# Performance work log

Hardware: AMD Instinct MI355X
Metric: run time of the kernel (lower is better)

The kernel has to match this reference:

```python
import jax, jax.numpy as jnp
import numpy as np

N_PARTICLES = 10_000_000
GRID_N = 256  # per-axis grid size
GRID_EDGE = 10.0  # grid spans [-10, 10] in each axis


def setup_inputs() -> dict:
    key = jax.random.key(0)
    k1, k2 = jax.random.split(key)
    # uniform in [-11, 11]: some particles fall outside the grid -> exercises bounds mask
    positions = jax.random.uniform(k1, (N_PARTICLES, 3), dtype=jnp.float32,
                                   minval=-11.0, maxval=11.0)
    weights = jax.random.uniform(k2, (N_PARTICLES,), dtype=jnp.float32)
    return {"positions": positions, "weights": weights}


def reference(positions, weights):
    # Grid buffers (from Grid.__init__ with grid_edges=(10,10,10), n=(256,256,256))
    n = GRID_N
    grid_min = jnp.full((3,), -GRID_EDGE, dtype=positions.dtype)
    grid_max = jnp.full((3,), GRID_EDGE, dtype=positions.dtype)
    dx = (grid_max - grid_min) / (n - 1)  # [3]

    # float index: fi = (pos - min)/dx  -> nearest grid point via trunc(fi + 0.5)
    fi = (positions - grid_min[None, :]) / dx[None, :]          # [N,3]
    i = (fi + 0.5).astype(jnp.int32)  # C-style trunc-toward-zero, matches torch .type(int64)

    gd = jnp.all((i >= 0) & (i < n), axis=1)                    # [N] in-grid mask

    # flatten 3D index; out-of-grid particles routed to index 0 with zero weight
    flat = (i[:, 0] * n + i[:, 1]) * n + i[:, 2]                # [N]
    flat = jnp.where(gd, flat, 0)
    w = jnp.where(gd, weights, jnp.zeros_like(weights))

    grid = jnp.zeros((n * n * n,), dtype=positions.dtype).at[flat].add(w)
    return grid.reshape(n, n, n)
```

## Files before the change

kernel.cpp:

```cpp
#include <hip/hip_runtime.h>
#include <stdint.h>


constexpr int GRID_N = 256;
constexpr int SB     = 1024;
constexpr int CELLS  = 16384;
constexpr int NB     = 256;
constexpr int BT     = 1024;
constexpr int RING   = 16;
constexpr int RSTR   = 17;
constexpr uint32_t SIDE_CAP = 65536;

typedef unsigned int u32x4 __attribute__((ext_vector_type(4)));
typedef float        f32x4 __attribute__((ext_vector_type(4)));

#define BAR_LGKM() do { \
    asm volatile("s_waitcnt lgkmcnt(0)" ::: "memory"); \
    __builtin_amdgcn_s_barrier(); \
} while (0)

__device__ __forceinline__ int particle_flat(float px, float py, float pz) {
#pragma clang fp contract(off)
    float fix = (px + 10.0f) * 12.75f;
    float fiy = (py + 10.0f) * 12.75f;
    float fiz = (pz + 10.0f) * 12.75f;
    int ix = (int)(fix + 0.5f);
    int iy = (int)(fiy + 0.5f);
    int iz = (int)(fiz + 0.5f);
    bool in = (ix >= 0) & (ix < GRID_N) &
              (iy >= 0) & (iy < GRID_N) &
              (iz >= 0) & (iz < GRID_N);
    return in ? ((ix << 16) | (iy << 8) | iz) : -1;
}

__global__ __launch_bounds__(1024) void k0_init(uint32_t* __restrict__ gcur,
                                                uint32_t* __restrict__ side_n,
                                                uint32_t C)
{
    int t = blockIdx.x * blockDim.x + threadIdx.x;
    if (t < SB) gcur[t] = (uint32_t)t * C;
    if (t == 0) *side_n = 0;
}

__global__ __launch_bounds__(BT, 1) void k3_direct(
    const float* __restrict__ pos, const float* __restrict__ wgt,
    uint32_t* __restrict__ gcur, uint2* __restrict__ pairs,
    uint2* __restrict__ side, uint32_t* __restrict__ side_n,
    uint32_t C, int n)
{
    __shared__ uint2    stg[SB][RSTR];
    __shared__ uint32_t s_total[SB];
    __shared__ uint32_t s_flushed[SB];
    __shared__ uint32_t s_wl[SB];
    __shared__ uint32_t s_wldst[SB];
    __shared__ uint32_t s_wln;

    const int tid = threadIdx.x;
    const int blk = blockIdx.x;

    s_total[tid]   = 0;
    s_flushed[tid] = 0;
    if (tid == 0) s_wln = 0;
    __syncthreads();

    const float4* p4 = (const float4*)pos;
    const float4* w4 = (const float4*)wgt;
    int ngroups = n >> 2;
    int G = NB * BT;
    int iters = (ngroups + G - 1) / G;

    int g = blk * BT + tid;
    bool valid = g < ngroups;
    float4 a = {}, b = {}, c = {}, w = {};
    if (valid) {
        a = p4[(size_t)g * 3 + 0];
        b = p4[(size_t)g * 3 + 1];
        c = p4[(size_t)g * 3 + 2];
        w = w4[g];
    }

    for (int it = 0; it < iters; ++it) {
        if (tid == 0) s_wln = 0;

        int gn = g + G;
        bool v2 = (it + 1 < iters) && (gn < ngroups);
        float4 a2 = {}, b2 = {}, c2 = {}, w2 = {};
        if (v2) {
            a2 = p4[(size_t)gn * 3 + 0];
            b2 = p4[(size_t)gn * 3 + 1];
            c2 = p4[(size_t)gn * 3 + 2];
            w2 = w4[gn];
        }

        if (valid) {
            int   f[4]  = { particle_flat(a.x, a.y, a.z), particle_flat(a.w, b.x, b.y),
                            particle_flat(b.z, b.w, c.x), particle_flat(c.y, c.z, c.w) };
            float ww[4] = { w.x, w.y, w.z, w.w };
#pragma unroll
            for (int k = 0; k < 4; ++k) {
                int fk = f[k];
                if (fk >= 0) {
                    uint32_t bin  = (uint32_t)fk >> 14;
                    uint32_t slot = atomicAdd(&s_total[bin], 1u);
                    if (slot - s_flushed[bin] < (uint32_t)RING) {
                        stg[bin][slot & (RING - 1)] =
                            make_uint2((uint32_t)fk & (CELLS - 1), __float_as_uint(ww[k]));
                    } else {
                        atomicSub(&s_total[bin], 1u);
                        uint32_t si = atomicAdd(side_n, 1u);
                        if (si < SIDE_CAP)
                            side[si] = make_uint2((uint32_t)fk, __float_as_uint(ww[k]));
                    }
                }
            }
        }
        BAR_LGKM();
        {
            uint32_t p = s_total[tid] - s_flushed[tid];
            if (p >= 8u) {
                uint32_t o   = s_flushed[tid];
                uint32_t dst = atomicAdd(&gcur[tid], 8u);
                if (dst + 8u <= (uint32_t)(tid + 1) * C) {
                    uint32_t wi = atomicAdd(&s_wln, 1u);
                    s_wl[wi]    = ((uint32_t)tid << 4) | (o & (RING - 1));
                    s_wldst[wi] = dst;
                } else {
                    atomicSub(&gcur[tid], 8u);
                    for (int j = 0; j < 8; ++j) {
                        uint2 v = stg[tid][(o + j) & (RING - 1)];
                        uint32_t si = atomicAdd(side_n, 1u);
                        if (si < SIDE_CAP)
                            side[si] = make_uint2(((uint32_t)tid << 14) | v.x, v.y);
                    }
                }
                s_flushed[tid] = o + 8u;
            }
        }
        BAR_LGKM();
        {
            uint32_t m = s_wln;
            for (uint32_t j = tid; j < m * 8u; j += BT) {
                uint32_t e = s_wl[j >> 3];
                uint2 v = stg[e >> 4][((e & (RING - 1)) + (j & 7u)) & (RING - 1)];
                uint64_t v64 = (uint64_t)v.x | ((uint64_t)v.y << 32);
                __builtin_nontemporal_store(v64,
                    (uint64_t*)&pairs[(size_t)s_wldst[j >> 3] + (j & 7u)]);
            }
        }
        BAR_LGKM();

        a = a2; b = b2; c = c2; w = w2; valid = v2; g = gn;
    }

    if (blk == 0 && tid == 0) {
        for (int p = n & ~3; p < n; ++p) {
            int f = particle_flat(pos[3 * p], pos[3 * p + 1], pos[3 * p + 2]);
            if (f >= 0) {
                uint32_t si = atomicAdd(side_n, 1u);
                if (si < SIDE_CAP)
                    side[si] = make_uint2((uint32_t)f, __float_as_uint(wgt[p]));
            }
        }
    }

    {
        uint32_t t = s_total[tid];
        uint32_t p = t - s_flushed[tid];
        uint32_t pad = ((p + 7u) & ~7u) - p;
        for (uint32_t j = 0; j < pad; ++j)
            stg[tid][(t + j) & (RING - 1)] = make_uint2(0u, 0u);
        s_total[tid] = t + pad;
    }
    __syncthreads();

    for (int r = 0; r < 2; ++r) {
        if (tid == 0) s_wln = 0;
        __syncthreads();
        {
            uint32_t p = s_total[tid] - s_flushed[tid];
            if (p >= 8u) {
                uint32_t o   = s_flushed[tid];
                uint32_t dst = atomicAdd(&gcur[tid], 8u);
                if (dst + 8u <= (uint32_t)(tid + 1) * C) {
                    uint32_t wi = atomicAdd(&s_wln, 1u);
                    s_wl[wi]    = ((uint32_t)tid << 4) | (o & (RING - 1));
                    s_wldst[wi] = dst;
                } else {
                    atomicSub(&gcur[tid], 8u);
                    for (int j = 0; j < 8; ++j) {
                        uint2 v = stg[tid][(o + j) & (RING - 1)];
                        uint32_t si = atomicAdd(side_n, 1u);
                        if (si < SIDE_CAP)
                            side[si] = make_uint2(((uint32_t)tid << 14) | v.x, v.y);
                    }
                }
                s_flushed[tid] = o + 8u;
            }
        }
        __syncthreads();
        {
            uint32_t m = s_wln;
            for (uint32_t j = tid; j < m * 8u; j += BT) {
                uint32_t e = s_wl[j >> 3];
                uint2 v = stg[e >> 4][((e & (RING - 1)) + (j & 7u)) & (RING - 1)];
                uint64_t v64 = (uint64_t)v.x | ((uint64_t)v.y << 32);
                __builtin_nontemporal_store(v64,
                    (uint64_t*)&pairs[(size_t)s_wldst[j >> 3] + (j & 7u)]);
            }
        }
        __syncthreads();
    }
}

__global__ __launch_bounds__(BT) void k4_direct(const uint2* __restrict__ pairs,
                                                const uint32_t* __restrict__ gcur,
                                                const uint2* __restrict__ side,
                                                const uint32_t* __restrict__ side_n,
                                                uint32_t C,
                                                float* __restrict__ grid)
{
    __shared__ float acc[CELLS];
    for (int i = threadIdx.x; i < CELLS; i += BT) acc[i] = 0.0f;
    __syncthreads();

    int b = blockIdx.x;
    uint32_t s = (uint32_t)b * C, e = gcur[b];
    const u32x4* pp = (const u32x4*)(pairs + s);
    uint32_t m = (e - s) >> 1;
    for (uint32_t i = threadIdx.x; i < m; i += BT) {
        u32x4 v = __builtin_nontemporal_load(&pp[i]);
        atomicAdd(&acc[v.x], __uint_as_float(v.y));
        atomicAdd(&acc[v.z], __uint_as_float(v.w));
    }
    uint32_t ns = *side_n;
    if (ns > SIDE_CAP) ns = SIDE_CAP;
    for (uint32_t i = threadIdx.x; i < ns; i += BT) {
        uint2 sv = side[i];
        if ((int)(sv.x >> 14) == b)
            atomicAdd(&acc[sv.x & (CELLS - 1)], __uint_as_float(sv.y));
    }
    __syncthreads();

    f32x4* out4 = (f32x4*)(grid + (size_t)b * CELLS);
    const f32x4* a4 = (const f32x4*)acc;
    for (int i = threadIdx.x; i < CELLS / 4; i += BT)
        __builtin_nontemporal_store(a4[i], &out4[i]);
}

__global__ __launch_bounds__(BT) void k1_hist(const float* __restrict__ pos,
                                              uint32_t* __restrict__ hist,
                                              int n)
{
    __shared__ uint32_t h[SB];
    for (int i = threadIdx.x; i < SB; i += BT) h[i] = 0;
    __syncthreads();

    const float4* p4 = (const float4*)pos;
    int ngroups = n >> 2;
    int G = gridDim.x * BT;
    for (int g = blockIdx.x * BT + threadIdx.x; g < ngroups; g += G) {
        float4 a = p4[(size_t)g * 3 + 0];
        float4 b = p4[(size_t)g * 3 + 1];
        float4 c = p4[(size_t)g * 3 + 2];
        int f0 = particle_flat(a.x, a.y, a.z);
        int f1 = particle_flat(a.w, b.x, b.y);
        int f2 = particle_flat(b.z, b.w, c.x);
        int f3 = particle_flat(c.y, c.z, c.w);
        if (f0 >= 0) atomicAdd(&h[f0 >> 14], 1u);
        if (f1 >= 0) atomicAdd(&h[f1 >> 14], 1u);
        if (f2 >= 0) atomicAdd(&h[f2 >> 14], 1u);
        if (f3 >= 0) atomicAdd(&h[f3 >> 14], 1u);
    }
    if (blockIdx.x == 0 && threadIdx.x == 0) {
        for (int p = n & ~3; p < n; ++p) {
            int f = particle_flat(pos[3 * p], pos[3 * p + 1], pos[3 * p + 2]);
            if (f >= 0) atomicAdd(&h[f >> 14], 1u);
        }
    }
    __syncthreads();
    uint32_t* out = hist + (size_t)blockIdx.x * SB;
    for (int i = threadIdx.x; i < SB; i += BT) out[i] = h[i];
}

__global__ __launch_bounds__(128) void k2a_colscan(const uint32_t* __restrict__ hist,
                                                   uint32_t* __restrict__ offs,
                                                   uint32_t* __restrict__ totals)
{
    int b = blockIdx.x * 128 + threadIdx.x;
    uint32_t run = 0;
    for (int blk = 0; blk < NB; blk += 8) {
        uint32_t v[8];
#pragma unroll
        for (int j = 0; j < 8; ++j)
            v[j] = hist[(size_t)(blk + j) * SB + b];
#pragma unroll
        for (int j = 0; j < 8; ++j) {
            offs[(size_t)(blk + j) * SB + b] = run;
            run += v[j];
        }
    }
    totals[b] = run;
}

__global__ __launch_bounds__(256) void k2b_scan(const uint32_t* __restrict__ totals,
                                                uint32_t* __restrict__ base)
{
    __shared__ uint32_t part[256];
    int t = threadIdx.x;
    uint32_t local[4];
    uint32_t s = 0;
#pragma unroll
    for (int j = 0; j < 4; ++j) { local[j] = totals[t * 4 + j]; s += local[j]; }
    part[t] = s;
    __syncthreads();
    if (t == 0) {
        uint32_t run = 0;
        for (int i = 0; i < 256; ++i) { uint32_t tmp = part[i]; part[i] = run; run += tmp; }
    }
    __syncthreads();
    uint32_t run = part[t];
#pragma unroll
    for (int j = 0; j < 4; ++j) { base[t * 4 + j] = run; run += local[j]; }
    if (t == 255) base[SB] = run;
}

__global__ __launch_bounds__(BT) void k3_scatter(const float* __restrict__ pos,
                                                 const float* __restrict__ wgt,
                                                 const uint32_t* __restrict__ offs,
                                                 const uint32_t* __restrict__ base,
                                                 uint2* __restrict__ pairs,
                                                 int n)
{
    __shared__ uint32_t cur[SB];
    for (int i = threadIdx.x; i < SB; i += BT)
        cur[i] = base[i] + offs[(size_t)blockIdx.x * SB + i];
    __syncthreads();

    const float4* p4 = (const float4*)pos;
    const float4* w4 = (const float4*)wgt;
    int ngroups = n >> 2;
    int G = gridDim.x * BT;
    for (int g = blockIdx.x * BT + threadIdx.x; g < ngroups; g += G) {
        float4 a = p4[(size_t)g * 3 + 0];
        float4 b = p4[(size_t)g * 3 + 1];
        float4 c = p4[(size_t)g * 3 + 2];
        float4 w = w4[g];
        int   f[4]  = { particle_flat(a.x, a.y, a.z), particle_flat(a.w, b.x, b.y),
                        particle_flat(b.z, b.w, c.x), particle_flat(c.y, c.z, c.w) };
        float ww[4] = { w.x, w.y, w.z, w.w };
#pragma unroll
        for (int k = 0; k < 4; ++k) {
            if (f[k] >= 0) {
                uint32_t slot = atomicAdd(&cur[f[k] >> 14], 1u);
                pairs[slot] = make_uint2((uint32_t)(f[k] & (CELLS - 1)),
                                         __float_as_uint(ww[k]));
            }
        }
    }
    if (blockIdx.x == 0 && threadIdx.x == 0) {
        for (int p = n & ~3; p < n; ++p) {
            int f = particle_flat(pos[3 * p], pos[3 * p + 1], pos[3 * p + 2]);
            if (f >= 0) {
                uint32_t slot = atomicAdd(&cur[f >> 14], 1u);
                pairs[slot] = make_uint2((uint32_t)(f & (CELLS - 1)),
                                         __float_as_uint(wgt[p]));
            }
        }
    }
}

__global__ __launch_bounds__(BT) void k4_seg(const uint2* __restrict__ pairs,
                                             const uint32_t* __restrict__ base,
                                             float* __restrict__ grid)
{
    __shared__ float acc[CELLS];
    for (int i = threadIdx.x; i < CELLS; i += BT) acc[i] = 0.0f;
    __syncthreads();

    int b = blockIdx.x;
    uint32_t s = base[b], e = base[b + 1];
    for (uint32_t i = s + threadIdx.x; i < e; i += BT) {
        uint2 p = pairs[i];
        atomicAdd(&acc[p.x], __uint_as_float(p.y));
    }
    __syncthreads();

    float4* out4 = (float4*)(grid + (size_t)b * CELLS);
    const float4* a4 = (const float4*)acc;
    for (int i = threadIdx.x; i < CELLS / 4; i += BT) out4[i] = a4[i];
}

__global__ __launch_bounds__(256) void forcegrid_scatter_atomic(
    const float* __restrict__ pos, const float* __restrict__ wgt,
    float* __restrict__ grid, int n)
{
    int t = blockIdx.x * blockDim.x + threadIdx.x;
    long long bse = (long long)t * 4;
    if (bse >= n) return;
    const float4* p4 = (const float4*)pos;
    float4 a = p4[(size_t)t * 3 + 0];
    float4 b = p4[(size_t)t * 3 + 1];
    float4 c = p4[(size_t)t * 3 + 2];
    float4 w = ((const float4*)wgt)[t];
    int   f[4]  = { particle_flat(a.x, a.y, a.z), particle_flat(a.w, b.x, b.y),
                    particle_flat(b.z, b.w, c.x), particle_flat(c.y, c.z, c.w) };
    float ww[4] = { w.x, w.y, w.z, w.w };
#pragma unroll
    for (int k = 0; k < 4; ++k) {
        if (bse + k >= n) break;
        if (f[k] >= 0) atomicAdd(&grid[f[k]], ww[k]);
    }
}

extern "C" void kernel_launch(void* const* d_in, const int* in_sizes, int n_in,
                              void* d_out, int out_size, void* d_ws, size_t ws_size,
                              hipStream_t stream)
{
    const float* pos = (const float*)d_in[0];
    const float* wgt = (const float*)d_in[1];
    float* grid = (float*)d_out;
    int n = in_sizes[0] / 3;

    uint32_t C = ((2u * (uint32_t)(n / SB) + 4096u) + 7u) & ~7u;
    if (C < 1024u) C = 1024u;
    size_t o1 = 0;
    uint2*    pairs1 = (uint2*)d_ws;                     o1 += (size_t)SB * C * sizeof(uint2);
    uint2*    side   = (uint2*)((char*)d_ws + o1);       o1 += (size_t)SIDE_CAP * sizeof(uint2);
    uint32_t* gcur   = (uint32_t*)((char*)d_ws + o1);    o1 += (size_t)SB * 4;
    uint32_t* side_n = (uint32_t*)((char*)d_ws + o1);    o1 += 64;

    if (ws_size >= o1) {
        k0_init  <<<1,  1024, 0, stream>>>(gcur, side_n, C);
        k3_direct<<<NB, BT,   0, stream>>>(pos, wgt, gcur, pairs1, side, side_n, C, n);
        k4_direct<<<SB, BT,   0, stream>>>(pairs1, gcur, side, side_n, C, grid);
        return;
    }

    size_t o2 = 0;
    uint2*    pairs2  = (uint2*)d_ws;                    o2 += (size_t)n * sizeof(uint2);
    uint32_t* hist2   = (uint32_t*)((char*)d_ws + o2);   o2 += (size_t)NB * SB * 4;
    uint32_t* offs2   = (uint32_t*)((char*)d_ws + o2);   o2 += (size_t)NB * SB * 4;
    uint32_t* totals2 = (uint32_t*)((char*)d_ws + o2);   o2 += (size_t)SB * 4;
    uint32_t* base2   = (uint32_t*)((char*)d_ws + o2);   o2 += (size_t)(SB + 1) * 4;

    if (ws_size >= o2) {
        k1_hist    <<<NB,       BT,  0, stream>>>(pos, hist2, n);
        k2a_colscan<<<SB / 128, 128, 0, stream>>>(hist2, offs2, totals2);
        k2b_scan   <<<1,        256, 0, stream>>>(totals2, base2);
        k3_scatter <<<NB,       BT,  0, stream>>>(pos, wgt, offs2, base2, pairs2, n);
        k4_seg     <<<SB,       BT,  0, stream>>>(pairs2, base2, grid);
    } else {
        (void)hipMemsetAsync(grid, 0, (size_t)out_size * sizeof(float), stream);
        int groups = (n + 3) / 4;
        forcegrid_scatter_atomic<<<(groups + 255) / 256, 256, 0, stream>>>(pos, wgt, grid, n);
    }
}
```

Measured before the change: 297.7 us.

## Use fixed per-(bin,block) pair segments instead of global atomic cursors

Each binning block now writes its staged pairs for each bin into a private fixed-capacity segment indexed by (bin, block), so no global atomic cursor is needed. Each thread flushes its own bin's ring directly with four 16-byte nontemporal stores, which removes the worklist and one barrier per iteration. Bin counts go to a cnt array that the accumulate kernel reads to walk its 256 segments, four threads per segment. Any overflow past CAP entries goes to the side buffer. This gives up compact contiguous segments, so the accumulate reads become more fragmented, and skewed inputs may spill heavily to the capped side list.

```diff
diff --git a/kernel.cpp b/kernel.cpp
--- a/kernel.cpp
+++ b/kernel.cpp
@@ -9,6 +9,7 @@
 constexpr int BT     = 1024;
 constexpr int RING   = 16;
 constexpr int RSTR   = 17;
+constexpr uint32_t CAP = 72;
 constexpr uint32_t SIDE_CAP = 65536;
 
 typedef unsigned int u32x4 __attribute__((ext_vector_type(4)));
@@ -33,35 +34,28 @@
     return in ? ((ix << 16) | (iy << 8) | iz) : -1;
 }
 
-__global__ __launch_bounds__(1024) void k0_init(uint32_t* __restrict__ gcur,
-                                                uint32_t* __restrict__ side_n,
-                                                uint32_t C)
-{
-    int t = blockIdx.x * blockDim.x + threadIdx.x;
-    if (t < SB) gcur[t] = (uint32_t)t * C;
-    if (t == 0) *side_n = 0;
+__global__ __launch_bounds__(64) void k0_init(uint32_t* __restrict__ side_n)
+{
+    if (threadIdx.x == 0) *side_n = 0;
 }
 
 __global__ __launch_bounds__(BT, 1) void k3_direct(
     const float* __restrict__ pos, const float* __restrict__ wgt,
-    uint32_t* __restrict__ gcur, uint2* __restrict__ pairs,
-    uint2* __restrict__ side, uint32_t* __restrict__ side_n,
-    uint32_t C, int n)
+    uint2* __restrict__ pairs, uint32_t* __restrict__ cnt,
+    uint2* __restrict__ side, uint32_t* __restrict__ side_n, int n)
 {
     __shared__ uint2    stg[SB][RSTR];
     __shared__ uint32_t s_total[SB];
     __shared__ uint32_t s_flushed[SB];
-    __shared__ uint32_t s_wl[SB];
-    __shared__ uint32_t s_wldst[SB];
-    __shared__ uint32_t s_wln;
 
     const int tid = threadIdx.x;
     const int blk = blockIdx.x;
 
     s_total[tid]   = 0;
     s_flushed[tid] = 0;
-    if (tid == 0) s_wln = 0;
-    __syncthreads();
+    __syncthreads();
+
+    const size_t segbase = ((size_t)tid * NB + blk) * CAP;
 
     const float4* p4 = (const float4*)pos;
     const float4* w4 = (const float4*)wgt;
@@ -80,8 +74,6 @@
     }
 
     for (int it = 0; it < iters; ++it) {
-        if (tid == 0) s_wln = 0;
-
         int gn = g + G;
         bool v2 = (it + 1 < iters) && (gn < ngroups);
         float4 a2 = {}, b2 = {}, c2 = {}, w2 = {};
@@ -116,36 +108,35 @@
         }
         BAR_LGKM();
         {
-            uint32_t p = s_total[tid] - s_flushed[tid];
-            if (p >= 8u) {
-                uint32_t o   = s_flushed[tid];
-                uint32_t dst = atomicAdd(&gcur[tid], 8u);
-                if (dst + 8u <= (uint32_t)(tid + 1) * C) {
-                    uint32_t wi = atomicAdd(&s_wln, 1u);
-                    s_wl[wi]    = ((uint32_t)tid << 4) | (o & (RING - 1));
-                    s_wldst[wi] = dst;
+            uint32_t t_ = s_total[tid];
+            uint32_t fl = s_flushed[tid];
+            while (t_ - fl >= 8u) {
+                uint32_t o = fl & (RING - 1);
+                if (fl < CAP) {
+                    uint2 v0 = stg[tid][o + 0], v1 = stg[tid][o + 1];
+                    uint2 v2r = stg[tid][o + 2], v3 = stg[tid][o + 3];
+                    uint2 v4 = stg[tid][o + 4], v5 = stg[tid][o + 5];
+                    uint2 v6 = stg[tid][o + 6], v7 = stg[tid][o + 7];
+                    u32x4 q0 = { v0.x, v0.y, v1.x, v1.y };
+                    u32x4 q1 = { v2r.x, v2r.y, v3.x, v3.y };
+                    u32x4 q2 = { v4.x, v4.y, v5.x, v5.y };
+                    u32x4 q3 = { v6.x, v6.y, v7.x, v7.y };
+                    u32x4* dst = (u32x4*)&pairs[segbase + fl];
+                    __builtin_nontemporal_store(q0, dst + 0);
+                    __builtin_nontemporal_store(q1, dst + 1);
+                    __builtin_nontemporal_store(q2, dst + 2);
+                    __builtin_nontemporal_store(q3, dst + 3);
                 } else {
-                    atomicSub(&gcur[tid], 8u);
                     for (int j = 0; j < 8; ++j) {
-                        uint2 v = stg[tid][(o + j) & (RING - 1)];
+                        uint2 v = stg[tid][o + j];
                         uint32_t si = atomicAdd(side_n, 1u);
                         if (si < SIDE_CAP)
                             side[si] = make_uint2(((uint32_t)tid << 14) | v.x, v.y);
                     }
                 }
-                s_flushed[tid] = o + 8u;
-            }
-        }
-        BAR_LGKM();
-        {
-            uint32_t m = s_wln;
-            for (uint32_t j = tid; j < m * 8u; j += BT) {
-                uint32_t e = s_wl[j >> 3];
-                uint2 v = stg[e >> 4][((e & (RING - 1)) + (j & 7u)) & (RING - 1)];
-                uint64_t v64 = (uint64_t)v.x | ((uint64_t)v.y << 32);
-                __builtin_nontemporal_store(v64,
-                    (uint64_t*)&pairs[(size_t)s_wldst[j >> 3] + (j & 7u)]);
-            }
+                fl += 8u;
+            }
+            s_flushed[tid] = fl;
         }
         BAR_LGKM();
 
@@ -164,73 +155,62 @@
     }
 
     {
-        uint32_t t = s_total[tid];
-        uint32_t p = t - s_flushed[tid];
-        uint32_t pad = ((p + 7u) & ~7u) - p;
-        for (uint32_t j = 0; j < pad; ++j)
-            stg[tid][(t + j) & (RING - 1)] = make_uint2(0u, 0u);
-        s_total[tid] = t + pad;
-    }
-    __syncthreads();
-
-    for (int r = 0; r < 2; ++r) {
-        if (tid == 0) s_wln = 0;
-        __syncthreads();
-        {
-            uint32_t p = s_total[tid] - s_flushed[tid];
-            if (p >= 8u) {
-                uint32_t o   = s_flushed[tid];
-                uint32_t dst = atomicAdd(&gcur[tid], 8u);
-                if (dst + 8u <= (uint32_t)(tid + 1) * C) {
-                    uint32_t wi = atomicAdd(&s_wln, 1u);
-                    s_wl[wi]    = ((uint32_t)tid << 4) | (o & (RING - 1));
-                    s_wldst[wi] = dst;
-                } else {
-                    atomicSub(&gcur[tid], 8u);
-                    for (int j = 0; j < 8; ++j) {
-                        uint2 v = stg[tid][(o + j) & (RING - 1)];
-                        uint32_t si = atomicAdd(side_n, 1u);
-                        if (si < SIDE_CAP)
-                            side[si] = make_uint2(((uint32_t)tid << 14) | v.x, v.y);
-                    }
+        uint32_t t_ = s_total[tid];
+        uint32_t fl = s_flushed[tid];
+        if (t_ > fl) {
+            uint32_t o = fl & (RING - 1);
+            if (fl < CAP) {
+                uint2 v0 = stg[tid][o + 0], v1 = stg[tid][o + 1];
+                uint2 v2r = stg[tid][o + 2], v3 = stg[tid][o + 3];
+                uint2 v4 = stg[tid][o + 4], v5 = stg[tid][o + 5];
+                uint2 v6 = stg[tid][o + 6], v7 = stg[tid][o + 7];
+                u32x4 q0 = { v0.x, v0.y, v1.x, v1.y };
+                u32x4 q1 = { v2r.x, v2r.y, v3.x, v3.y };
+                u32x4 q2 = { v4.x, v4.y, v5.x, v5.y };
+                u32x4 q3 = { v6.x, v6.y, v7.x, v7.y };
+                u32x4* dst = (u32x4*)&pairs[segbase + fl];
+                __builtin_nontemporal_store(q0, dst + 0);
+                __builtin_nontemporal_store(q1, dst + 1);
+                __builtin_nontemporal_store(q2, dst + 2);
+                __builtin_nontemporal_store(q3, dst + 3);
+            } else {
+                for (uint32_t j = 0; j < t_ - fl; ++j) {
+                    uint2 v = stg[tid][(o + j) & (RING - 1)];
+                    uint32_t si = atomicAdd(side_n, 1u);
+                    if (si < SIDE_CAP)
+                        side[si] = make_uint2(((uint32_t)tid << 14) | v.x, v.y);
                 }
-                s_flushed[tid] = o + 8u;
-            }
-        }
-        __syncthreads();
-        {
-            uint32_t m = s_wln;
-            for (uint32_t j = tid; j < m * 8u; j += BT) {
-                uint32_t e = s_wl[j >> 3];
-                uint2 v = stg[e >> 4][((e & (RING - 1)) + (j & 7u)) & (RING - 1)];
-                uint64_t v64 = (uint64_t)v.x | ((uint64_t)v.y << 32);
-                __builtin_nontemporal_store(v64,
-                    (uint64_t*)&pairs[(size_t)s_wldst[j >> 3] + (j & 7u)]);
-            }
-        }
-        __syncthreads();
+            }
+        }
+        cnt[(size_t)tid * NB + blk] = t_ < CAP ? t_ : CAP;
     }
 }
 
 __global__ __launch_bounds__(BT) void k4_direct(const uint2* __restrict__ pairs,
-                                                const uint32_t* __restrict__ gcur,
+                                                const uint32_t* __restrict__ cnt,
                                                 const uint2* __restrict__ side,
                                                 const uint32_t* __restrict__ side_n,
-                                                uint32_t C,
                                                 float* __restrict__ grid)
 {
-    __shared__ float acc[CELLS];
+    __shared__ float    acc[CELLS];
+    __shared__ uint32_t s_cnt[NB];
+
+    int b = blockIdx.x;
+    if (threadIdx.x < NB) s_cnt[threadIdx.x] = cnt[(size_t)b * NB + threadIdx.x];
     for (int i = threadIdx.x; i < CELLS; i += BT) acc[i] = 0.0f;
     __syncthreads();
 
-    int b = blockIdx.x;
-    uint32_t s = (uint32_t)b * C, e = gcur[b];
-    const u32x4* pp = (const u32x4*)(pairs + s);
-    uint32_t m = (e - s) >> 1;
-    for (uint32_t i = threadIdx.x; i < m; i += BT) {
-        u32x4 v = __builtin_nontemporal_load(&pp[i]);
-        atomicAdd(&acc[v.x], __uint_as_float(v.y));
-        atomicAdd(&acc[v.z], __uint_as_float(v.w));
+    {
+        int seg = threadIdx.x >> 2;
+        int q   = threadIdx.x & 3;
+        uint32_t c = s_cnt[seg];
+        const u32x4* base = (const u32x4*)&pairs[((size_t)b * NB + seg) * CAP];
+        for (uint32_t p0 = (uint32_t)q * 2u; p0 < c; p0 += 8u) {
+            u32x4 v = __builtin_nontemporal_load(base + (p0 >> 1));
+            atomicAdd(&acc[v.x & (CELLS - 1)], __uint_as_float(v.y));
+            if (p0 + 1u < c)
+                atomicAdd(&acc[v.z & (CELLS - 1)], __uint_as_float(v.w));
+        }
     }
     uint32_t ns = *side_n;
     if (ns > SIDE_CAP) ns = SIDE_CAP;
@@ -421,18 +401,16 @@
     float* grid = (float*)d_out;
     int n = in_sizes[0] / 3;
 
-    uint32_t C = ((2u * (uint32_t)(n / SB) + 4096u) + 7u) & ~7u;
-    if (C < 1024u) C = 1024u;
     size_t o1 = 0;
-    uint2*    pairs1 = (uint2*)d_ws;                     o1 += (size_t)SB * C * sizeof(uint2);
+    uint2*    pairs1 = (uint2*)d_ws;                     o1 += (size_t)SB * NB * CAP * sizeof(uint2);
+    uint32_t* cnt    = (uint32_t*)((char*)d_ws + o1);    o1 += (size_t)SB * NB * 4;
     uint2*    side   = (uint2*)((char*)d_ws + o1);       o1 += (size_t)SIDE_CAP * sizeof(uint2);
-    uint32_t* gcur   = (uint32_t*)((char*)d_ws + o1);    o1 += (size_t)SB * 4;
     uint32_t* side_n = (uint32_t*)((char*)d_ws + o1);    o1 += 64;
 
-    if (ws_size >= o1) {
-        k0_init  <<<1,  1024, 0, stream>>>(gcur, side_n, C);
-        k3_direct<<<NB, BT,   0, stream>>>(pos, wgt, gcur, pairs1, side, side_n, C, n);
-        k4_direct<<<SB, BT,   0, stream>>>(pairs1, gcur, side, side_n, C, grid);
+    if (ws_size >= o1 && n >= 4) {
+        k0_init  <<<1,  64, 0, stream>>>(side_n);
+        k3_direct<<<NB, BT, 0, stream>>>(pos, wgt, pairs1, cnt, side, side_n, n);
+        k4_direct<<<SB, BT, 0, stream>>>(pairs1, cnt, side, side_n, grid);
         return;
     }
 
```

Result: slower. 372.7 us (+25.2%).
